# Kernel tuning notes

Hardware: AMD Instinct MI355X
Metric: run time of the kernel (lower is better)

The kernel has to match this reference:

```python
import jax, jax.numpy as jnp
import numpy as np

BS = 128      # batch
L = 512       # encoder sequence length
ENC = 512     # enc_hs
DEC = 1024    # dec_hs
ATTN = 512    # attn_sz
EMB = 256     # emb_sz
VOCAB = 128   # alphabet_size
MAX_LEN = 128 # text_max_len
SOS = 0


def setup_inputs() -> dict:
    key = jax.random.key(0)
    ks = jax.random.split(key, 10)
    s = 0.02
    return {
        "enc_out": jax.random.normal(ks[0], (BS, ENC, L), jnp.float32),
        # attention.encoder_conv (Conv1d enc->attn, kernel 1 == matmul)
        "W_enc": jax.random.normal(ks[1], (ATTN, ENC), jnp.float32) * s,
        "b_enc": jnp.zeros((ATTN,), jnp.float32),
        # attention.decoder_linear
        "W_dec": jax.random.normal(ks[2], (ATTN, DEC), jnp.float32) * s,
        "b_dec": jnp.zeros((ATTN,), jnp.float32),
        # attention.energy_layer (Conv1d attn->1, kernel 1)
        "v_e": jax.random.normal(ks[3], (ATTN,), jnp.float32) * s,
        "b_e": jnp.zeros((), jnp.float32),
        # embedding table
        "emb_table": jax.random.normal(ks[4], (VOCAB, EMB), jnp.float32) * s,
        # LSTM (single layer), PyTorch gate order i,f,g,o
        "W_ih": jax.random.normal(ks[5], (4 * DEC, EMB + ENC), jnp.float32) * s,
        "W_hh": jax.random.normal(ks[6], (4 * DEC, DEC), jnp.float32) * s,
        "b_ih": jnp.zeros((4 * DEC,), jnp.float32),
        "b_hh": jnp.zeros((4 * DEC,), jnp.float32),
        # output projection
        "W_out": jax.random.normal(ks[7], (VOCAB, DEC), jnp.float32) * s,
        "b_out": jnp.zeros((VOCAB,), jnp.float32),
    }


def reference(enc_out, W_enc, b_enc, W_dec, b_dec, v_e, b_e, emb_table,
              W_ih, W_hh, b_ih, b_hh, W_out, b_out):
    bs = enc_out.shape[0]
    # encoder_conv applied once: [bs, attn, L]
    weighted_enc = jnp.einsum('ae,bel->bal', W_enc, enc_out) + b_enc[None, :, None]

    def step(carry, _):
        x_idx, h, c = carry
        emb_x = emb_table[x_idx]                                   # [bs, emb]
        # Bahdanau attention
        wdec = h @ W_dec.T + b_dec                                 # [bs, attn]
        pre = jnp.tanh(weighted_enc + wdec[:, :, None])            # [bs, attn, L]
        scores = jnp.einsum('bal,a->bl', pre, v_e) + b_e           # [bs, L]
        alphas = jax.nn.softmax(scores, axis=-1)                   # [bs, L]
        context = jnp.einsum('bel,bl->be', enc_out, alphas)        # [bs, enc]
        # LSTM cell (PyTorch gate order i, f, g, o)
        rnn_x = jnp.concatenate([emb_x, context], axis=1)          # [bs, emb+enc]
        gates = rnn_x @ W_ih.T + b_ih + h @ W_hh.T + b_hh          # [bs, 4*dec]
        i, f, g, o = jnp.split(gates, 4, axis=1)
        i = jax.nn.sigmoid(i); f = jax.nn.sigmoid(f)
        g = jnp.tanh(g); o = jax.nn.sigmoid(o)
        c_new = f * c + i * g
        h_new = o * jnp.tanh(c_new)
        logits = h_new @ W_out.T + b_out                           # [bs, vocab]
        logp = jax.nn.log_softmax(logits, axis=-1)
        next_word = jnp.argmax(logp, axis=1).astype(jnp.int32)
        return (next_word, h_new, c_new), (logp, next_word, alphas)

    x0 = jnp.full((bs,), SOS, dtype=jnp.int32)
    h0 = jnp.zeros((bs, DEC), enc_out.dtype)
    c0 = jnp.zeros((bs, DEC), enc_out.dtype)
    _, (logp, preds, attn) = jax.lax.scan(step, (x0, h0, c0), None, length=MAX_LEN)
    # [T,bs,*] -> [bs,T,*]
    return logp.transpose(1, 0, 2), preds.transpose(1, 0), attn.transpose(1, 0, 2)
```

## Files before the change

### kernel.cpp

```cpp
#include <hip/hip_runtime.h>
#include <math.h>

#define BS 128
#define L 512
#define ENC 512
#define DEC 1024
#define ATTN 512
#define EMB 256
#define VOCAB 128
#define TMAX 128
#define KCAT 1792
#define G4 4096

#define OFF_WET    0ull
#define OFF_WGR    33554432ull
#define OFF_BGR    40894464ull
#define OFF_WOUTT  40898560ull
#define OFF_WDT    41029632ull
#define OFF_C      41553920ull
#define OFF_SC     41684992ull
#define OFF_FLAG   41750528ull
#define OFF_XCAT   41816064ull
#define OFF_GPART  42045440ull

__device__ __forceinline__ float tanh_fast(float x) {
    float ax = fabsf(x);
    float e = __expf(-2.f * ax);
    float d = 1.f + e;
    float r = __builtin_amdgcn_rcpf(d);
    r = r * (2.f - d * r);
    float t = 1.f - 2.f * e * r;
    return copysignf(t, x);
}

__device__ __forceinline__ void pairsync(int* flag, int target) {
    __syncthreads();
    if (threadIdx.x == 0) {
        __threadfence();
        __hip_atomic_fetch_add(flag, 1, __ATOMIC_ACQ_REL, __HIP_MEMORY_SCOPE_AGENT);
        while (__hip_atomic_load(flag, __ATOMIC_RELAXED, __HIP_MEMORY_SCOPE_AGENT) < target) {
            __builtin_amdgcn_s_sleep(4);
        }
        __threadfence();
    }
    __syncthreads();
}

__global__ void k_prep(const float* __restrict__ W_ih, const float* __restrict__ W_hh,
                       const float* __restrict__ b_ih, const float* __restrict__ b_hh,
                       const float* __restrict__ W_out, const float* __restrict__ W_dec,
                       float* __restrict__ Wgr, float* __restrict__ bgr,
                       float* __restrict__ WoutT, float* __restrict__ WdT) {
    long i = (long)blockIdx.x * 256 + threadIdx.x;
    if (i < (long)G4 * KCAT) {
        int mp = (int)(i / KCAT), k = (int)(i % KCAT);
        int d = mp >> 2, g = mp & 3;
        int r = g * DEC + d;
        Wgr[i] = (k < EMB + ENC) ? W_ih[(long)r * (EMB + ENC) + k]
                                 : W_hh[(long)r * DEC + (k - (EMB + ENC))];
        return;
    }
    long j = i - (long)G4 * KCAT;
    if (j < G4) {
        int d = (int)(j >> 2), g = (int)(j & 3);
        int r = g * DEC + d;
        bgr[j] = b_ih[r] + b_hh[r];
        return;
    }
    long m = j - G4;
    if (m < (long)DEC * VOCAB) {
        int k = (int)(m / VOCAB), v = (int)(m % VOCAB);
        WoutT[m] = W_out[(long)v * DEC + k];
        return;
    }
    long p = m - (long)DEC * VOCAB;
    if (p < (long)DEC * ATTN) {
        int k = (int)(p / ATTN), a = (int)(p % ATTN);
        WdT[p] = W_dec[(long)a * DEC + k];
    }
}

__global__ void k_init(const float* __restrict__ emb_table,
                       float* __restrict__ c, float* __restrict__ Xcat,
                       int* __restrict__ flags) {
    long i = (long)blockIdx.x * 256 + threadIdx.x;
    if (i < BS * 16) flags[i] = 0;
    if (i < BS * DEC) { c[i] = 0.f; return; }
    long j = i - BS * DEC;
    if (j < (long)BS * KCAT) {
        int cdx = (int)(j % KCAT);
        Xcat[j] = (cdx < EMB) ? emb_table[cdx] : 0.f;
    }
}

__global__ __launch_bounds__(256) void k_wenc(const float* __restrict__ W_enc,
                                              const float* __restrict__ b_enc,
                                              const float* __restrict__ enc_out,
                                              float* __restrict__ weT) {
    __shared__ float As[16][68];
    __shared__ float Bs[16][68];
    int b = blockIdx.z;
    int a0 = blockIdx.y * 64;
    int l0 = blockIdx.x * 64;
    int t = threadIdx.x;
    int ty = t >> 4, tx = t & 15;
    float acc[4][4] = {};
    for (int e0 = 0; e0 < ENC; e0 += 16) {
        {
            int ar = t >> 2;
            int kg = (t & 3) << 2;
            float4 w4 = *(const float4*)&W_enc[(size_t)(a0 + ar) * ENC + e0 + kg];
            As[kg + 0][ar] = w4.x; As[kg + 1][ar] = w4.y; As[kg + 2][ar] = w4.z; As[kg + 3][ar] = w4.w;
            int er = t >> 4;
            int lg = (t & 15) << 2;
            float4 x4 = *(const float4*)&enc_out[((size_t)b * ENC + e0 + er) * L + l0 + lg];
            *(float4*)&Bs[er][lg] = x4;
        }
        __syncthreads();
        #pragma unroll
        for (int kk = 0; kk < 16; kk++) {
            float4 a4 = *(const float4*)&As[kk][ty * 4];
            float4 x4 = *(const float4*)&Bs[kk][tx * 4];
            float av[4] = {a4.x, a4.y, a4.z, a4.w};
            float xv[4] = {x4.x, x4.y, x4.z, x4.w};
            #pragma unroll
            for (int i = 0; i < 4; i++)
                #pragma unroll
                for (int j = 0; j < 4; j++) acc[i][j] += av[i] * xv[j];
        }
        __syncthreads();
    }
    float be0 = b_enc[a0 + ty * 4 + 0];
    float be1 = b_enc[a0 + ty * 4 + 1];
    float be2 = b_enc[a0 + ty * 4 + 2];
    float be3 = b_enc[a0 + ty * 4 + 3];
    #pragma unroll
    for (int j = 0; j < 4; j++) {
        int l = l0 + tx * 4 + j;
        float4 o = {acc[0][j] + be0, acc[1][j] + be1, acc[2][j] + be2, acc[3][j] + be3};
        *(float4*)&weT[((size_t)b * L + l) * ATTN + a0 + ty * 4] = o;
    }
}

__global__ __launch_bounds__(512) void k_aof(const float* __restrict__ gpart,
                                             const float* __restrict__ bgr,
                                             const float* __restrict__ WoutT,
                                             const float* __restrict__ b_out,
                                             const float* __restrict__ emb_table,
                                             const float* __restrict__ WdT,
                                             const float* __restrict__ b_dec,
                                             float* __restrict__ c,
                                             float* __restrict__ logp_out,
                                             float* __restrict__ preds_out,
                                             float* __restrict__ Xcat,
                                             const float* __restrict__ weT,
                                             const float* __restrict__ v_e,
                                             const float* __restrict__ b_e,
                                             const float* __restrict__ enc_out,
                                             float* __restrict__ attn_out,
                                             float* __restrict__ sc_g,
                                             int* __restrict__ flags, int ts) {
    __shared__ float hs[DEC];
    __shared__ float wd[ATTN];
    __shared__ float ve[ATTN];
    __shared__ float al[L];
    __shared__ float red[512];
    __shared__ float rv[128];
    __shared__ int ri[128];
    __shared__ float scl[256];
    int b = blockIdx.x >> 1, h = blockIdx.x & 1;
    int t = threadIdx.x;
    int* flag = flags + b * 16;
    int msync = (ts == 0) ? 0 : (2 * ts - 1);

    if (ts > 0) {
        float cold0 = c[(size_t)b * DEC + t];
        float cold1 = c[(size_t)b * DEC + 512 + t];
        pairsync(flag, 2 * (++msync));
        #pragma unroll
        for (int q = 0; q < 2; q++) {
            int d = q * 512 + t;
            const float* gp = gpart + (size_t)b * G4 + d * 4;
            float4 g = *(const float4*)gp;
            #pragma unroll
            for (int ks = 1; ks < 4; ks++) {
                float4 p = *(const float4*)(gp + (size_t)ks * BS * G4);
                g.x += p.x; g.y += p.y; g.z += p.z; g.w += p.w;
            }
            float4 bb = *(const float4*)&bgr[(size_t)d * 4];
            float gi = g.x + bb.x, gf = g.y + bb.y, gg = g.z + bb.z, go = g.w + bb.w;
            float fi = 1.f / (1.f + expf(-gi));
            float ff = 1.f / (1.f + expf(-gf));
            float fg = tanhf(gg);
            float fo = 1.f / (1.f + expf(-go));
            float cold = q ? cold1 : cold0;
            float cn = ff * cold + fi * fg;
            float hn = fo * tanhf(cn);
            if (h == 0) {
                c[(size_t)b * DEC + d] = cn;
                Xcat[(size_t)b * KCAT + EMB + ENC + d] = hn;
            }
            hs[d] = hn;
        }
        __syncthreads();
        if (h == 0) {
            int v = t & 127, kh = t >> 7;
            const float* wp = WoutT + (size_t)kh * 256 * VOCAB + v;
            float acc = 0.f;
            #pragma unroll 8
            for (int k = 0; k < 256; k++) acc += wp[(size_t)k * VOCAB] * hs[kh * 256 + k];
            red[t] = acc;
            __syncthreads();
            float logits = 0.f;
            if (t < 128) {
                logits = ((red[t] + red[t + 128]) + (red[t + 256] + red[t + 384])) + b_out[t];
                rv[t] = logits; ri[t] = t;
            }
            __syncthreads();
            for (int s = 64; s; s >>= 1) {
                if (t < s) {
                    float ov = rv[t + s]; int oi = ri[t + s];
                    if (ov > rv[t] || (ov == rv[t] && oi < ri[t])) { rv[t] = ov; ri[t] = oi; }
                }
                __syncthreads();
            }
            float m = rv[0]; int am = ri[0];
            __syncthreads();
            if (t < 128) red[t] = expf(logits - m);
            __syncthreads();
            for (int s = 64; s; s >>= 1) { if (t < s && t + s < 128) red[t] += red[t + s]; __syncthreads(); }
            if (t < 128) logp_out[((size_t)b * TMAX + (ts - 1)) * VOCAB + t] = logits - m - logf(red[0]);
            if (t == 0) preds_out[(size_t)b * TMAX + (ts - 1)] = (float)am;
            if (t < 256) Xcat[(size_t)b * KCAT + t] = emb_table[(size_t)am * EMB + t];
        }
        {
            const float* wdp = WdT + t;
            float s = 0.f;
            #pragma unroll 16
            for (int k = 0; k < DEC; k++) s += wdp[(size_t)k * ATTN] * hs[k];
            wd[t] = s + b_dec[t];
        }
        if (ts == TMAX) return;
    } else {
        wd[t] = b_dec[t];
    }
    ve[t] = v_e[t];
    __syncthreads();

    {
        int r2 = t >> 1, ah = t & 1;
        int l = h * 256 + r2;
        const float* row = weT + ((size_t)b * L + l) * ATTN + ah * 256;
        float acc = 0.f;
        #pragma unroll 8
        for (int a4 = 0; a4 < 256; a4 += 4) {
            float4 x = *(const float4*)&row[a4];
            int a = ah * 256 + a4;
            acc += ve[a + 0] * tanh_fast(x.x + wd[a + 0]);
            acc += ve[a + 1] * tanh_fast(x.y + wd[a + 1]);
            acc += ve[a + 2] * tanh_fast(x.z + wd[a + 2]);
            acc += ve[a + 3] * tanh_fast(x.w + wd[a + 3]);
        }
        acc += __shfl_xor(acc, 1, 64);
        if (ah == 0) {
            float s = acc + b_e[0];
            scl[r2] = s;
            sc_g[(size_t)b * L + l] = s;
        }
    }
    pairsync(flag, 2 * (++msync));

    float sc;
    if (t >= h * 256 && t < h * 256 + 256) sc = scl[t - h * 256];
    else sc = sc_g[(size_t)b * L + t];
    red[t] = sc;
    __syncthreads();
    for (int s = 256; s; s >>= 1) { if (t < s) red[t] = fmaxf(red[t], red[t + s]); __syncthreads(); }
    float m = red[0];
    __syncthreads();
    float e = expf(sc - m);
    red[t] = e;
    __syncthreads();
    for (int s = 256; s; s >>= 1) { if (t < s) red[t] += red[t + s]; __syncthreads(); }
    float inv = 1.f / red[0];
    al[t] = e * inv;
    __syncthreads();
    if (h == 0) attn_out[((size_t)b * TMAX + ts) * L + t] = al[t];

    {
        int r2 = t >> 1, lh2 = (t & 1) * 256;
        int e_ = h * 256 + r2;
        const float* erow = enc_out + ((size_t)b * ENC + e_) * L + lh2;
        float cacc = 0.f;
        #pragma unroll 8
        for (int l4 = 0; l4 < 256; l4 += 4) {
            float4 x = *(const float4*)&erow[l4];
            float4 a4 = *(const float4*)&al[lh2 + l4];
            cacc += x.x * a4.x + x.y * a4.y + x.z * a4.z + x.w * a4.w;
        }
        cacc += __shfl_xor(cacc, 1, 64);
        if ((t & 1) == 0) Xcat[(size_t)b * KCAT + EMB + e_] = cacc;
    }
}

__global__ __launch_bounds__(256) void k_gates(const float* __restrict__ Wgr,
                                               const float* __restrict__ Xcat,
                                               float* __restrict__ gates_part) {
    __shared__ float As[16][68];
    __shared__ float Xs[16][36];
    int M0 = blockIdx.x * 64;
    int b0 = blockIdx.y * 32;
    int ks = blockIdx.z;
    int kbase = ks * 448, kend = kbase + 448;
    int t = threadIdx.x, ty = t >> 4, tx = t & 15;
    int r = t >> 2, kg = (t & 3) << 2;
    float acc[4][2] = {};
    float4 wreg = *(const float4*)&Wgr[(size_t)(M0 + r) * KCAT + kbase + kg];
    float4 xreg;
    if (t < 128) xreg = *(const float4*)&Xcat[(size_t)(b0 + r) * KCAT + kbase + kg];
    for (int k0 = kbase; k0 < kend; k0 += 16) {
        As[kg + 0][r] = wreg.x; As[kg + 1][r] = wreg.y; As[kg + 2][r] = wreg.z; As[kg + 3][r] = wreg.w;
        if (t < 128) {
            Xs[kg + 0][r] = xreg.x; Xs[kg + 1][r] = xreg.y; Xs[kg + 2][r] = xreg.z; Xs[kg + 3][r] = xreg.w;
        }
        __syncthreads();
        if (k0 + 16 < kend) {
            wreg = *(const float4*)&Wgr[(size_t)(M0 + r) * KCAT + k0 + 16 + kg];
            if (t < 128) xreg = *(const float4*)&Xcat[(size_t)(b0 + r) * KCAT + k0 + 16 + kg];
        }
        #pragma unroll
        for (int kk = 0; kk < 16; kk++) {
            float4 a4 = *(const float4*)&As[kk][ty * 4];
            float xb0 = Xs[kk][tx * 2], xb1 = Xs[kk][tx * 2 + 1];
            acc[0][0] += a4.x * xb0; acc[0][1] += a4.x * xb1;
            acc[1][0] += a4.y * xb0; acc[1][1] += a4.y * xb1;
            acc[2][0] += a4.z * xb0; acc[2][1] += a4.z * xb1;
            acc[3][0] += a4.w * xb0; acc[3][1] += a4.w * xb1;
        }
        __syncthreads();
    }
    float* gp = gates_part + (size_t)ks * BS * G4;
    #pragma unroll
    for (int j = 0; j < 2; j++) {
        float4 o = {acc[0][j], acc[1][j], acc[2][j], acc[3][j]};
        *(float4*)&gp[(size_t)(b0 + tx * 2 + j) * G4 + M0 + ty * 4] = o;
    }
}

extern "C" void kernel_launch(void* const* d_in, const int* in_sizes, int n_in,
                              void* d_out, int out_size, void* d_ws, size_t ws_size,
                              hipStream_t stream) {
    const float* enc_out = (const float*)d_in[0];
    const float* W_enc   = (const float*)d_in[1];
    const float* b_enc   = (const float*)d_in[2];
    const float* W_dec   = (const float*)d_in[3];
    const float* b_dec   = (const float*)d_in[4];
    const float* v_e     = (const float*)d_in[5];
    const float* b_e     = (const float*)d_in[6];
    const float* emb     = (const float*)d_in[7];
    const float* W_ih    = (const float*)d_in[8];
    const float* W_hh    = (const float*)d_in[9];
    const float* b_ih    = (const float*)d_in[10];
    const float* b_hh    = (const float*)d_in[11];
    const float* W_out   = (const float*)d_in[12];
    const float* b_out   = (const float*)d_in[13];

    float* ws    = (float*)d_ws;
    float* weT   = ws + OFF_WET;
    float* Wgr   = ws + OFF_WGR;
    float* bgr   = ws + OFF_BGR;
    float* WoutT = ws + OFF_WOUTT;
    float* WdT   = ws + OFF_WDT;
    float* c     = ws + OFF_C;
    float* sc_g  = ws + OFF_SC;
    int*   flags = (int*)(ws + OFF_FLAG);
    float* Xcat  = ws + OFF_XCAT;
    float* gpart = ws + OFF_GPART;

    float* logp_out  = (float*)d_out;
    float* preds_out = logp_out + (size_t)BS * TMAX * VOCAB;
    float* attn_out  = preds_out + (size_t)BS * TMAX;

    {
        long n = (long)G4 * KCAT + G4 + (long)DEC * VOCAB + (long)DEC * ATTN;
        k_prep<<<(int)((n + 255) / 256), 256, 0, stream>>>(W_ih, W_hh, b_ih, b_hh, W_out, W_dec,
                                                           Wgr, bgr, WoutT, WdT);
    }
    {
        long n = (long)BS * DEC + (long)BS * KCAT;
        k_init<<<(int)((n + 255) / 256), 256, 0, stream>>>(emb, c, Xcat, flags);
    }
    k_wenc<<<dim3(8, 8, 128), 256, 0, stream>>>(W_enc, b_enc, enc_out, weT);

    for (int t = 0; t < TMAX; t++) {
        k_aof<<<256, 512, 0, stream>>>(gpart, bgr, WoutT, b_out, emb, WdT, b_dec, c,
                                       logp_out, preds_out, Xcat, weT, v_e, b_e,
                                       enc_out, attn_out, sc_g, flags, t);
        k_gates<<<dim3(64, 4, 4), 256, 0, stream>>>(Wgr, Xcat, gpart);
    }
    k_aof<<<256, 512, 0, stream>>>(gpart, bgr, WoutT, b_out, emb, WdT, b_dec, c,
                                   logp_out, preds_out, Xcat, weT, v_e, b_e,
                                   enc_out, attn_out, sc_g, flags, TMAX);
}
```

Before: 20.49 ms.

## Split attention kernel across four blocks per batch row along attn dimension

The per-step attention kernel now uses four blocks per batch element instead of two. Each block handles a 128-wide slice of the attention dimension for all 512 positions, writes partial scores to global memory, and the four partials are summed after a 4-way inter-block flag sync. The decoder-linear projection is also split per quarter with a 4-way k-split reduction in shared memory, which removes the redundant full wdec computation each block used to do. This doubles the grid to 512 blocks for better CU occupancy, at the cost of more blocks spinning on global atomics, extra partial-score traffic, and the LSTM gate recompute now being repeated in four blocks.

Result: slower. 26.76 ms (+30.6%).

```diff
diff --git a/kernel.cpp b/kernel.cpp
--- a/kernel.cpp
+++ b/kernel.cpp
@@ -18,10 +18,10 @@
 #define OFF_WOUTT  40898560ull
 #define OFF_WDT    41029632ull
 #define OFF_C      41553920ull
-#define OFF_SC     41684992ull
-#define OFF_FLAG   41750528ull
+#define OFF_FLAG   41684992ull
 #define OFF_XCAT   41816064ull
 #define OFF_GPART  42045440ull
+#define OFF_SCP    44142592ull
 
 __device__ __forceinline__ float tanh_fast(float x) {
     float ax = fabsf(x);
@@ -33,7 +33,7 @@
     return copysignf(t, x);
 }
 
-__device__ __forceinline__ void pairsync(int* flag, int target) {
+__device__ __forceinline__ void gsync(int* flag, int target) {
     __syncthreads();
     if (threadIdx.x == 0) {
         __threadfence();
@@ -158,17 +158,17 @@
                                              const float* __restrict__ b_e,
                                              const float* __restrict__ enc_out,
                                              float* __restrict__ attn_out,
-                                             float* __restrict__ sc_g,
+                                             float* __restrict__ scp,
                                              int* __restrict__ flags, int ts) {
     __shared__ float hs[DEC];
-    __shared__ float wd[ATTN];
-    __shared__ float ve[ATTN];
+    __shared__ float wd_l[128];
+    __shared__ float vel[128];
     __shared__ float al[L];
     __shared__ float red[512];
     __shared__ float rv[128];
     __shared__ int ri[128];
-    __shared__ float scl[256];
-    int b = blockIdx.x >> 1, h = blockIdx.x & 1;
+    __shared__ float redw[128][4];
+    int b = blockIdx.x >> 2, q = blockIdx.x & 3;
     int t = threadIdx.x;
     int* flag = flags + b * 16;
     int msync = (ts == 0) ? 0 : (2 * ts - 1);
@@ -176,10 +176,10 @@
     if (ts > 0) {
         float cold0 = c[(size_t)b * DEC + t];
         float cold1 = c[(size_t)b * DEC + 512 + t];
-        pairsync(flag, 2 * (++msync));
+        gsync(flag, 4 * (++msync));
         #pragma unroll
-        for (int q = 0; q < 2; q++) {
-            int d = q * 512 + t;
+        for (int q2 = 0; q2 < 2; q2++) {
+            int d = q2 * 512 + t;
             const float* gp = gpart + (size_t)b * G4 + d * 4;
             float4 g = *(const float4*)gp;
             #pragma unroll
@@ -193,17 +193,17 @@
             float ff = 1.f / (1.f + expf(-gf));
             float fg = tanhf(gg);
             float fo = 1.f / (1.f + expf(-go));
-            float cold = q ? cold1 : cold0;
+            float cold = q2 ? cold1 : cold0;
             float cn = ff * cold + fi * fg;
             float hn = fo * tanhf(cn);
-            if (h == 0) {
+            if (q == 0) {
                 c[(size_t)b * DEC + d] = cn;
                 Xcat[(size_t)b * KCAT + EMB + ENC + d] = hn;
             }
             hs[d] = hn;
         }
         __syncthreads();
-        if (h == 0) {
+        if (q == 0) {
             int v = t & 127, kh = t >> 7;
             const float* wp = WoutT + (size_t)kh * 256 * VOCAB + v;
             float acc = 0.f;
@@ -233,46 +233,49 @@
             if (t == 0) preds_out[(size_t)b * TMAX + (ts - 1)] = (float)am;
             if (t < 256) Xcat[(size_t)b * KCAT + t] = emb_table[(size_t)am * EMB + t];
         }
+        if (ts == TMAX) return;
         {
-            const float* wdp = WdT + t;
+            int a_l = t >> 2, ksub = t & 3;
+            int a = q * 128 + a_l;
+            const float* wdp = WdT + (size_t)(ksub * 256) * ATTN + a;
             float s = 0.f;
-            #pragma unroll 16
-            for (int k = 0; k < DEC; k++) s += wdp[(size_t)k * ATTN] * hs[k];
-            wd[t] = s + b_dec[t];
-        }
-        if (ts == TMAX) return;
+            #pragma unroll 8
+            for (int k = 0; k < 256; k++) s += wdp[(size_t)k * ATTN] * hs[ksub * 256 + k];
+            redw[a_l][ksub] = s;
+        }
+        __syncthreads();
+        if (t < 128) {
+            wd_l[t] = ((redw[t][0] + redw[t][1]) + (redw[t][2] + redw[t][3])) + b_dec[q * 128 + t];
+            vel[t] = v_e[q * 128 + t];
+        }
     } else {
-        wd[t] = b_dec[t];
-    }
-    ve[t] = v_e[t];
+        if (t < 128) {
+            wd_l[t] = b_dec[q * 128 + t];
+            vel[t] = v_e[q * 128 + t];
+        }
+    }
     __syncthreads();
 
     {
-        int r2 = t >> 1, ah = t & 1;
-        int l = h * 256 + r2;
-        const float* row = weT + ((size_t)b * L + l) * ATTN + ah * 256;
+        const float* row = weT + ((size_t)b * L + t) * ATTN + q * 128;
         float acc = 0.f;
         #pragma unroll 8
-        for (int a4 = 0; a4 < 256; a4 += 4) {
+        for (int a4 = 0; a4 < 128; a4 += 4) {
             float4 x = *(const float4*)&row[a4];
-            int a = ah * 256 + a4;
-            acc += ve[a + 0] * tanh_fast(x.x + wd[a + 0]);
-            acc += ve[a + 1] * tanh_fast(x.y + wd[a + 1]);
-            acc += ve[a + 2] * tanh_fast(x.z + wd[a + 2]);
-            acc += ve[a + 3] * tanh_fast(x.w + wd[a + 3]);
-        }
-        acc += __shfl_xor(acc, 1, 64);
-        if (ah == 0) {
-            float s = acc + b_e[0];
-            scl[r2] = s;
-            sc_g[(size_t)b * L + l] = s;
-        }
-    }
-    pairsync(flag, 2 * (++msync));
-
-    float sc;
-    if (t >= h * 256 && t < h * 256 + 256) sc = scl[t - h * 256];
-    else sc = sc_g[(size_t)b * L + t];
+            acc += vel[a4 + 0] * tanh_fast(x.x + wd_l[a4 + 0]);
+            acc += vel[a4 + 1] * tanh_fast(x.y + wd_l[a4 + 1]);
+            acc += vel[a4 + 2] * tanh_fast(x.z + wd_l[a4 + 2]);
+            acc += vel[a4 + 3] * tanh_fast(x.w + wd_l[a4 + 3]);
+        }
+        scp[((size_t)q * BS + b) * L + t] = acc;
+    }
+    gsync(flag, 4 * (++msync));
+
+    float sc = scp[((size_t)0 * BS + b) * L + t]
+             + scp[((size_t)1 * BS + b) * L + t]
+             + scp[((size_t)2 * BS + b) * L + t]
+             + scp[((size_t)3 * BS + b) * L + t]
+             + b_e[0];
     red[t] = sc;
     __syncthreads();
     for (int s = 256; s; s >>= 1) { if (t < s) red[t] = fmaxf(red[t], red[t + s]); __syncthreads(); }
@@ -285,21 +288,22 @@
     float inv = 1.f / red[0];
     al[t] = e * inv;
     __syncthreads();
-    if (h == 0) attn_out[((size_t)b * TMAX + ts) * L + t] = al[t];
+    if (q == 0) attn_out[((size_t)b * TMAX + ts) * L + t] = al[t];
 
     {
-        int r2 = t >> 1, lh2 = (t & 1) * 256;
-        int e_ = h * 256 + r2;
-        const float* erow = enc_out + ((size_t)b * ENC + e_) * L + lh2;
+        int r2 = t >> 2, lq = (t & 3) * 128;
+        int e_ = q * 128 + r2;
+        const float* erow = enc_out + ((size_t)b * ENC + e_) * L + lq;
         float cacc = 0.f;
         #pragma unroll 8
-        for (int l4 = 0; l4 < 256; l4 += 4) {
+        for (int l4 = 0; l4 < 128; l4 += 4) {
             float4 x = *(const float4*)&erow[l4];
-            float4 a4 = *(const float4*)&al[lh2 + l4];
+            float4 a4 = *(const float4*)&al[lq + l4];
             cacc += x.x * a4.x + x.y * a4.y + x.z * a4.z + x.w * a4.w;
         }
         cacc += __shfl_xor(cacc, 1, 64);
-        if ((t & 1) == 0) Xcat[(size_t)b * KCAT + EMB + e_] = cacc;
+        cacc += __shfl_xor(cacc, 2, 64);
+        if ((t & 3) == 0) Xcat[(size_t)b * KCAT + EMB + e_] = cacc;
     }
 }
 
@@ -372,10 +376,10 @@
     float* WoutT = ws + OFF_WOUTT;
     float* WdT   = ws + OFF_WDT;
     float* c     = ws + OFF_C;
-    float* sc_g  = ws + OFF_SC;
     int*   flags = (int*)(ws + OFF_FLAG);
     float* Xcat  = ws + OFF_XCAT;
     float* gpart = ws + OFF_GPART;
+    float* scp   = ws + OFF_SCP;
 
     float* logp_out  = (float*)d_out;
     float* preds_out = logp_out + (size_t)BS * TMAX * VOCAB;
@@ -393,12 +397,12 @@
     k_wenc<<<dim3(8, 8, 128), 256, 0, stream>>>(W_enc, b_enc, enc_out, weT);
 
     for (int t = 0; t < TMAX; t++) {
-        k_aof<<<256, 512, 0, stream>>>(gpart, bgr, WoutT, b_out, emb, WdT, b_dec, c,
+        k_aof<<<512, 512, 0, stream>>>(gpart, bgr, WoutT, b_out, emb, WdT, b_dec, c,
                                        logp_out, preds_out, Xcat, weT, v_e, b_e,
-                                       enc_out, attn_out, sc_g, flags, t);
+                                       enc_out, attn_out, scp, flags, t);
         k_gates<<<dim3(64, 4, 4), 256, 0, stream>>>(Wgr, Xcat, gpart);
     }
-    k_aof<<<256, 512, 0, stream>>>(gpart, bgr, WoutT, b_out, emb, WdT, b_dec, c,
+    k_aof<<<512, 512, 0, stream>>>(gpart, bgr, WoutT, b_out, emb, WdT, b_dec, c,
                                    logp_out, preds_out, Xcat, weT, v_e, b_e,
-                                   enc_out, attn_out, sc_g, flags, TMAX);
-}
+                                   enc_out, attn_out, scp, flags, TMAX);
+}
```

## Split attention work across block pair by attn dimension instead of sequence

Applied to the files above, without the earlier changes.

Each of the two blocks per batch row now computes wdec for only its half of the attention dimension, splitting the K=1024 reduction across thread pairs, and then computes partial energy scores over all 512 positions for that half. The two partial score arrays are summed after the pair sync. This halves the redundant W_dec matvec that each block previously did over the full attention size. The cost is that every block now reads scores from global memory for all positions instead of half. The flag buffer is also moved to make room for the doubled score buffer.

Result: no change. 20.66 ms (+0.8%).

```diff
diff --git a/kernel.cpp b/kernel.cpp
--- a/kernel.cpp
+++ b/kernel.cpp
@@ -18,10 +18,10 @@
 #define OFF_WOUTT  40898560ull
 #define OFF_WDT    41029632ull
 #define OFF_C      41553920ull
-#define OFF_SC     41684992ull
-#define OFF_FLAG   41750528ull
+#define OFF_SCP    41684992ull
 #define OFF_XCAT   41816064ull
 #define OFF_GPART  42045440ull
+#define OFF_FLAG   44142592ull
 
 __device__ __forceinline__ float tanh_fast(float x) {
     float ax = fabsf(x);
@@ -158,16 +158,16 @@
                                              const float* __restrict__ b_e,
                                              const float* __restrict__ enc_out,
                                              float* __restrict__ attn_out,
-                                             float* __restrict__ sc_g,
+                                             float* __restrict__ scp,
                                              int* __restrict__ flags, int ts) {
     __shared__ float hs[DEC];
-    __shared__ float wd[ATTN];
-    __shared__ float ve[ATTN];
+    __shared__ float wd_l[256];
+    __shared__ float vel[256];
     __shared__ float al[L];
     __shared__ float red[512];
     __shared__ float rv[128];
     __shared__ int ri[128];
-    __shared__ float scl[256];
+    __shared__ float redw[256][2];
     int b = blockIdx.x >> 1, h = blockIdx.x & 1;
     int t = threadIdx.x;
     int* flag = flags + b * 16;
@@ -233,46 +233,52 @@
             if (t == 0) preds_out[(size_t)b * TMAX + (ts - 1)] = (float)am;
             if (t < 256) Xcat[(size_t)b * KCAT + t] = emb_table[(size_t)am * EMB + t];
         }
+        if (ts == TMAX) return;
         {
-            const float* wdp = WdT + t;
+            int a_l = t >> 1, ksub = t & 1;
+            int a = h * 256 + a_l;
+            const float* wdp = WdT + (size_t)(ksub * 512) * ATTN + a;
             float s = 0.f;
             #pragma unroll 16
-            for (int k = 0; k < DEC; k++) s += wdp[(size_t)k * ATTN] * hs[k];
-            wd[t] = s + b_dec[t];
-        }
-        if (ts == TMAX) return;
+            for (int k = 0; k < 512; k++) s += wdp[(size_t)k * ATTN] * hs[ksub * 512 + k];
+            redw[a_l][ksub] = s;
+        }
+        __syncthreads();
+        if (t < 256) {
+            wd_l[t] = (redw[t][0] + redw[t][1]) + b_dec[h * 256 + t];
+            vel[t] = v_e[h * 256 + t];
+        }
     } else {
-        wd[t] = b_dec[t];
-    }
-    ve[t] = v_e[t];
+        if (t < 256) {
+            wd_l[t] = b_dec[h * 256 + t];
+            vel[t] = v_e[h * 256 + t];
+        }
+    }
     __syncthreads();
 
     {
-        int r2 = t >> 1, ah = t & 1;
-        int l = h * 256 + r2;
-        const float* row = weT + ((size_t)b * L + l) * ATTN + ah * 256;
-        float acc = 0.f;
-        #pragma unroll 8
-        for (int a4 = 0; a4 < 256; a4 += 4) {
-            float4 x = *(const float4*)&row[a4];
-            int a = ah * 256 + a4;
-            acc += ve[a + 0] * tanh_fast(x.x + wd[a + 0]);
-            acc += ve[a + 1] * tanh_fast(x.y + wd[a + 1]);
-            acc += ve[a + 2] * tanh_fast(x.z + wd[a + 2]);
-            acc += ve[a + 3] * tanh_fast(x.w + wd[a + 3]);
-        }
-        acc += __shfl_xor(acc, 1, 64);
-        if (ah == 0) {
-            float s = acc + b_e[0];
-            scl[r2] = s;
-            sc_g[(size_t)b * L + l] = s;
+        int ah = t & 1;
+        #pragma unroll
+        for (int rr = 0; rr < 2; rr++) {
+            int l = rr * 256 + (t >> 1);
+            const float* row = weT + ((size_t)b * L + l) * ATTN + h * 256 + ah * 128;
+            float acc = 0.f;
+            #pragma unroll 8
+            for (int a4 = 0; a4 < 128; a4 += 4) {
+                float4 x = *(const float4*)&row[a4];
+                int a = ah * 128 + a4;
+                acc += vel[a + 0] * tanh_fast(x.x + wd_l[a + 0]);
+                acc += vel[a + 1] * tanh_fast(x.y + wd_l[a + 1]);
+                acc += vel[a + 2] * tanh_fast(x.z + wd_l[a + 2]);
+                acc += vel[a + 3] * tanh_fast(x.w + wd_l[a + 3]);
+            }
+            acc += __shfl_xor(acc, 1, 64);
+            if (ah == 0) scp[((size_t)h * BS + b) * L + l] = acc;
         }
     }
     pairsync(flag, 2 * (++msync));
 
-    float sc;
-    if (t >= h * 256 && t < h * 256 + 256) sc = scl[t - h * 256];
-    else sc = sc_g[(size_t)b * L + t];
+    float sc = scp[(size_t)b * L + t] + scp[((size_t)BS + b) * L + t] + b_e[0];
     red[t] = sc;
     __syncthreads();
     for (int s = 256; s; s >>= 1) { if (t < s) red[t] = fmaxf(red[t], red[t + s]); __syncthreads(); }
@@ -372,10 +378,10 @@
     float* WoutT = ws + OFF_WOUTT;
     float* WdT   = ws + OFF_WDT;
     float* c     = ws + OFF_C;
-    float* sc_g  = ws + OFF_SC;
-    int*   flags = (int*)(ws + OFF_FLAG);
+    float* scp   = ws + OFF_SCP;
     float* Xcat  = ws + OFF_XCAT;
     float* gpart = ws + OFF_GPART;
+    int*   flags = (int*)(ws + OFF_FLAG);
 
     float* logp_out  = (float*)d_out;
     float* preds_out = logp_out + (size_t)BS * TMAX * VOCAB;
@@ -395,10 +401,10 @@
     for (int t = 0; t < TMAX; t++) {
         k_aof<<<256, 512, 0, stream>>>(gpart, bgr, WoutT, b_out, emb, WdT, b_dec, c,
                                        logp_out, preds_out, Xcat, weT, v_e, b_e,
-                                       enc_out, attn_out, sc_g, flags, t);
+                                       enc_out, attn_out, scp, flags, t);
         k_gates<<<dim3(64, 4, 4), 256, 0, stream>>>(Wgr, Xcat, gpart);
     }
     k_aof<<<256, 512, 0, stream>>>(gpart, bgr, WoutT, b_out, emb, WdT, b_dec, c,
                                    logp_out, preds_out, Xcat, weT, v_e, b_e,
-                                   enc_out, attn_out, sc_g, flags, TMAX);
-}
+                                   enc_out, attn_out, scp, flags, TMAX);
+}
```
